# Performance work log

Hardware: AMD Instinct MI355X
Metric: run time of the kernel (lower is better)

Reference implementation:

```python
import jax, jax.numpy as jnp
import numpy as np

LAM = 0.43
IN_DIM = 256
BATCH = 512


def _persistence_pairs(D):
    """0-dim persistence pairs via Kruskal-style union-find (matches torch code).
    D: [n, n] numpy distance matrix. Returns [n-1, 2] int array of MST edges."""
    n = D.shape[0]
    parent = np.arange(n)

    def find(u):
        root = u
        while parent[root] != root:
            root = parent[root]
        while parent[u] != root:  # path compression
            parent[u], u = root, parent[u]
        return root

    iu, ju = np.triu_indices(n)  # includes diagonal, like triu_indices_from
    w = D[iu, ju]
    order = np.argsort(w, kind='stable')
    pairs = []
    for e in order:
        u, v = int(iu[e]), int(ju[e])
        ru, rv = find(u), find(v)
        if ru == rv:
            continue
        if ru > rv:
            parent[rv] = ru  # merge(v, u)
        else:
            parent[ru] = rv  # merge(u, v)
        pairs.append((u, v) if u < v else (v, u))
    return np.asarray(pairs, dtype=np.int64)  # exactly n-1 edges


def _pdist(x):
    # torch.norm(x[:, None] - x, dim=2, p=2)
    return jnp.linalg.norm(x[:, None, :] - x[None, :, :], axis=-1)


def setup_inputs() -> dict:
    key = jax.random.key(0)
    ks = jax.random.split(key, 16)
    d = IN_DIM
    dims = [(d, d // 2), (d // 2, d // 4), (d // 4, 2), (2, d // 4), (d // 4, d // 2), (d // 2, d)]
    inp = {
        'x': jax.random.normal(ks[0], (BATCH, d), dtype=jnp.float32),
        'label': jax.random.randint(ks[1], (BATCH,), 0, 10),
    }
    names = ['1', '2', 'm', '3', '4', '5']
    for i, (nm, (din, dout)) in enumerate(zip(names, dims)):
        s = 1.0 / np.sqrt(din)
        inp['W' + nm] = jax.random.uniform(ks[2 + 2 * i], (din, dout), minval=-s, maxval=s, dtype=jnp.float32)
        inp['b' + nm] = jax.random.uniform(ks[3 + 2 * i], (dout,), minval=-s, maxval=s, dtype=jnp.float32)
    inp['latent_norm'] = jnp.ones((1,), dtype=jnp.float32)
    return inp


def reference(x, label, W1, b1, W2, b2, Wm, bm, W3, b3, W4, b4, W5, b5, latent_norm):
    # Encoder
    h1 = jax.nn.relu(x @ W1 + b1)
    h2 = jax.nn.relu(h1 @ W2 + b2)
    lat = h2 @ Wm + bm  # [B, 2]

    # normalized pairwise distance matrices
    xd = _pdist(x)
    xd = xd / xd.max()  # 2D-input branch
    ld = _pdist(lat) / latent_norm[0]

    # Decoder
    h3 = jax.nn.relu(lat @ W3 + b3)
    h4 = jax.nn.relu(h3 @ W4 + b4)
    xr = h4 @ W5 + b5
    ae_loss = jnp.mean((x - xr) ** 2)

    # persistence pairs (detached / host computation, as in the torch code)
    p1 = _persistence_pairs(np.asarray(jax.device_get(xd)))
    p2 = _persistence_pairs(np.asarray(jax.device_get(ld)))

    sig1 = xd[p1[:, 0], p1[:, 1]]
    sig1_2 = ld[p1[:, 0], p1[:, 1]]
    sig2 = ld[p2[:, 0], p2[:, 1]]
    sig2_1 = xd[p2[:, 0], p2[:, 1]]
    topo = jnp.sum((sig1 - sig1_2) ** 2) + jnp.sum((sig2 - sig2_1) ** 2)

    loss = ae_loss + LAM * topo / float(x.shape[0])
    return loss
```

## Files before the change

kernel.cpp:

```cpp
#include <hip/hip_runtime.h>
#include <math.h>

#define N      512
#define DIN    256
#define LAM    0.43f
#define MAGIC  0x4D535431u
#define NBW    64
#define PAD(j) ((j) + (((j) >> 6) << 2))

#define OFF_LDREADY 4
#define OFF_T0READY 5
#define OFF_T0BITS  6
#define OFF_BLKMAX  8
#define OFF_AEPART  128
#define OFF_LAT     1024
#define OFF_XD      2048
#define OFF_LD      (2048 + 262144)
#define OFF_CAND    526336
#define OFF_GCOMP   (OFF_CAND + 2048)
#define OFF_GNC     (OFF_GCOMP + 1024)
#define OFF_DBAR    (OFF_GNC + 16)
#define OFF_SBAR    (OFF_DBAR + 32)
#define OFF_LDBAR   (OFF_SBAR + 1280)

__device__ __forceinline__ unsigned ld_acq(unsigned* p) {
    return __hip_atomic_load(p, __ATOMIC_ACQUIRE, __HIP_MEMORY_SCOPE_AGENT);
}
__device__ __forceinline__ void st_rel(unsigned* p, unsigned v) {
    __hip_atomic_store(p, v, __ATOMIC_RELEASE, __HIP_MEMORY_SCOPE_AGENT);
}
__device__ __forceinline__ unsigned ld_rlx(unsigned* p) {
    return __hip_atomic_load(p, __ATOMIC_RELAXED, __HIP_MEMORY_SCOPE_AGENT);
}
__device__ __forceinline__ void st_rlx(unsigned* p, unsigned v) {
    __hip_atomic_store(p, v, __ATOMIC_RELAXED, __HIP_MEMORY_SCOPE_AGENT);
}
__device__ __forceinline__ unsigned long long ld64_rlx(unsigned long long* p) {
    return __hip_atomic_load(p, __ATOMIC_RELAXED, __HIP_MEMORY_SCOPE_AGENT);
}
__device__ __forceinline__ void st64_rlx(unsigned long long* p, unsigned long long v) {
    __hip_atomic_store(p, v, __ATOMIC_RELAXED, __HIP_MEMORY_SCOPE_AGENT);
}
__device__ __forceinline__ void spin_magic(unsigned* p) {
    while (ld_acq(p) != MAGIC) __builtin_amdgcn_s_sleep(1);
}

__global__ __launch_bounds__(256) void fused_mlp_pdistx_kernel(
    const float* __restrict__ x,
    const float* __restrict__ W1, const float* __restrict__ b1,
    const float* __restrict__ W2, const float* __restrict__ b2,
    const float* __restrict__ Wm, const float* __restrict__ bm,
    const float* __restrict__ W3, const float* __restrict__ b3,
    const float* __restrict__ W4, const float* __restrict__ b4,
    const float* __restrict__ W5, const float* __restrict__ b5,
    float* __restrict__ lat_out, float* __restrict__ ae_part,
    float* __restrict__ xd, float* __restrict__ blkmax)
{
    const int tid = threadIdx.x;

    if (blockIdx.x < 512) {
        __shared__ float xs[256];
        __shared__ float h1[128];
        __shared__ float h2[64];
        __shared__ float latv[2];
        __shared__ float h3[64];
        __shared__ float h4[128];
        __shared__ float red[4];

        const int row = blockIdx.x;
        xs[tid] = x[(size_t)row * DIN + tid];
        __syncthreads();

        if (tid < 128) {
            float s = b1[tid];
            for (int k = 0; k < 256; ++k) s = fmaf(xs[k], W1[k * 128 + tid], s);
            h1[tid] = fmaxf(s, 0.f);
        }
        __syncthreads();

        if (tid < 64) {
            float s = b2[tid];
            for (int k = 0; k < 128; ++k) s = fmaf(h1[k], W2[k * 64 + tid], s);
            h2[tid] = fmaxf(s, 0.f);
        }
        __syncthreads();

        if (tid < 2) {
            float s = bm[tid];
            for (int k = 0; k < 64; ++k) s = fmaf(h2[k], Wm[k * 2 + tid], s);
            latv[tid] = s;
            lat_out[(size_t)row * 2 + tid] = s;
        }
        __syncthreads();

        if (tid < 64) {
            float s = b3[tid];
            s = fmaf(latv[0], W3[tid], s);
            s = fmaf(latv[1], W3[64 + tid], s);
            h3[tid] = fmaxf(s, 0.f);
        }
        __syncthreads();

        if (tid < 128) {
            float s = b4[tid];
            for (int k = 0; k < 64; ++k) s = fmaf(h3[k], W4[k * 128 + tid], s);
            h4[tid] = fmaxf(s, 0.f);
        }
        __syncthreads();

        float s = b5[tid];
        for (int k = 0; k < 128; ++k) s = fmaf(h4[k], W5[k * 256 + tid], s);
        float diff = xs[tid] - s;
        float a = diff * diff;

        #pragma unroll
        for (int m = 1; m < 64; m <<= 1) a += __shfl_xor(a, m, 64);
        if ((tid & 63) == 0) red[tid >> 6] = a;
        __syncthreads();
        if (tid == 0) ae_part[row] = red[0] + red[1] + red[2] + red[3];
    } else {
        __shared__ float As[32][65];
        __shared__ float Bs[32][65];
        __shared__ float red2[4];

        const int bid = blockIdx.x - 512;
        const int bi = bid & 7, bj = bid >> 3;
        const int i0 = bi * 64, j0 = bj * 64;
        const int ty = tid >> 4, tx = tid & 15;

        float acc[4][4];
        #pragma unroll
        for (int i = 0; i < 4; ++i)
            #pragma unroll
            for (int j = 0; j < 4; ++j) acc[i][j] = 0.f;

        for (int kk = 0; kk < DIN; kk += 32) {
            #pragma unroll
            for (int s = tid; s < 512; s += 256) {
                int r = s >> 3, c4 = (s & 7) << 2;
                float4 va = *(const float4*)(x + (size_t)(i0 + r) * DIN + kk + c4);
                As[c4 + 0][r] = va.x; As[c4 + 1][r] = va.y;
                As[c4 + 2][r] = va.z; As[c4 + 3][r] = va.w;
                float4 vb = *(const float4*)(x + (size_t)(j0 + r) * DIN + kk + c4);
                Bs[c4 + 0][r] = vb.x; Bs[c4 + 1][r] = vb.y;
                Bs[c4 + 2][r] = vb.z; Bs[c4 + 3][r] = vb.w;
            }
            __syncthreads();
            #pragma unroll 8
            for (int k = 0; k < 32; ++k) {
                float a[4], b[4];
                #pragma unroll
                for (int i = 0; i < 4; ++i) a[i] = As[k][ty + 16 * i];
                #pragma unroll
                for (int j = 0; j < 4; ++j) b[j] = Bs[k][tx + 16 * j];
                #pragma unroll
                for (int i = 0; i < 4; ++i)
                    #pragma unroll
                    for (int j = 0; j < 4; ++j) {
                        float d = a[i] - b[j];
                        acc[i][j] = fmaf(d, d, acc[i][j]);
                    }
            }
            __syncthreads();
        }

        float lmax = 0.f;
        #pragma unroll
        for (int i = 0; i < 4; ++i)
            #pragma unroll
            for (int j = 0; j < 4; ++j) {
                float dd = sqrtf(acc[i][j]);
                int r = i0 + ty + 16 * i, c = j0 + tx + 16 * j;
                xd[(size_t)r * N + c] = dd;
                lmax = fmaxf(lmax, dd);
            }

        #pragma unroll
        for (int m = 32; m >= 1; m >>= 1) lmax = fmaxf(lmax, __shfl_xor(lmax, m, 64));
        if ((tid & 63) == 0) red2[tid >> 6] = lmax;
        __syncthreads();
        if (tid == 0)
            blkmax[bid] = fmaxf(fmaxf(red2[0], red2[1]), fmaxf(red2[2], red2[3]));
    }
}

__global__ __launch_bounds__(256) void mst_boruvka_kernel(
    const float* __restrict__ xd, float* __restrict__ ld,
    const float* __restrict__ lat, const float* __restrict__ latent_norm,
    const float* __restrict__ blkmax, const float* __restrict__ ae_part,
    float* __restrict__ wsf, float* __restrict__ out)
{
    __shared__ __align__(16) unsigned comp_p[544];
    __shared__ unsigned comp_a[512];
    __shared__ unsigned long long cval[512];
    __shared__ int tgt[512];
    __shared__ unsigned short eu[512], ev[512];
    __shared__ float ew[512];
    __shared__ float latx[512], laty[512];
    __shared__ float s_red[4];
    __shared__ float s_xdm;
    __shared__ int s_ecnt;
    __shared__ unsigned s_nc;

    const int tid = threadIdx.x;
    const int blk = blockIdx.x;
    const int m   = blk >> 6;
    const int wb  = blk & 63;
    const bool leader = (wb == 0);

    unsigned* ldready = (unsigned*)(wsf + OFF_LDREADY);
    unsigned* t0ready = (unsigned*)(wsf + OFF_T0READY);
    unsigned* t0bits  = (unsigned*)(wsf + OFF_T0BITS);
    unsigned long long* cand = (unsigned long long*)(wsf + OFF_CAND) + (size_t)m * 512;
    unsigned* gcomp = (unsigned*)(wsf + OFF_GCOMP) + (size_t)m * 512;
    unsigned* gnc   = (unsigned*)(wsf + OFF_GNC) + m;
    unsigned* dbar  = (unsigned*)(wsf + OFF_DBAR) + (size_t)m * 16;
    unsigned* sbar  = (unsigned*)(wsf + OFF_SBAR) + (size_t)m * 640;
    unsigned* ldbar = (unsigned*)(wsf + OFF_LDBAR);

    const float* Dm = m ? ld : xd;
    const float* Om = m ? xd : ld;

    if (m == 1) {
        for (int i = tid; i < 512; i += 256) {
            latx[i] = lat[2 * i + 0];
            laty[i] = lat[2 * i + 1];
        }
        __syncthreads();
        const int r0 = wb << 3;
        for (int q = tid; q < 1024; q += 256) {
            int rr = r0 + (q >> 7);
            int j  = (q & 127) << 2;
            float xi = latx[rr], yi = laty[rr];
            float dx0 = xi - latx[j + 0], dy0 = yi - laty[j + 0];
            float dx1 = xi - latx[j + 1], dy1 = yi - laty[j + 1];
            float dx2 = xi - latx[j + 2], dy2 = yi - laty[j + 2];
            float dx3 = xi - latx[j + 3], dy3 = yi - laty[j + 3];
            float4 o;
            o.x = sqrtf(fmaf(dx0, dx0, dy0 * dy0));
            o.y = sqrtf(fmaf(dx1, dx1, dy1 * dy1));
            o.z = sqrtf(fmaf(dx2, dx2, dy2 * dy2));
            o.w = sqrtf(fmaf(dx3, dx3, dy3 * dy3));
            *(float4*)(ld + (size_t)rr * N + j) = o;
        }
        __syncthreads();
        if (tid == 0) st_rel(&ldbar[wb], MAGIC);
        if (tid < 64) spin_magic(&ldbar[tid]);
        __syncthreads();
        if (leader && tid == 0) st_rel(ldready, MAGIC);
    }

    if (leader) {
        for (int i = tid; i < 512; i += 256) comp_a[i] = (unsigned)i;
        if (tid == 0) s_ecnt = 0;
        for (int i = tid; i < 512; i += 256) st64_rlx(&cand[i], ~0ULL);
        __syncthreads();
        if (tid == 0) st_rel(&dbar[0], MAGIC);
    }
    if (tid == 0) spin_magic(&dbar[0]);
    __syncthreads();

    for (int p = 0; p < 9; ++p) {
        if (p > 0) {
            if (tid == 0) { spin_magic(&dbar[p]); s_nc = ld_rlx(gnc); }
            __syncthreads();
            if (s_nc == 1) break;
            for (int i = tid; i < 512; i += 256)
                comp_p[PAD(i)] = ld_rlx(&gcomp[i]);
            __syncthreads();
        }

        const int r  = (wb << 3) + (tid >> 5);
        const int c0 = (tid & 31) << 4;
        const unsigned cv = (p == 0) ? (unsigned)r : comp_p[PAD(r)];
        const float4* rp = (const float4*)(Dm + (size_t)r * N + c0);
        const int4*   cp = (const int4*)&comp_p[PAD(c0)];
        unsigned long long bk = ~0ULL;
        #pragma unroll
        for (int c = 0; c < 4; ++c) {
            float4 f = rp[c];
            int jb = c0 + 4 * c;
            unsigned j0c, j1c, j2c, j3c;
            if (p == 0) { j0c = jb; j1c = jb + 1; j2c = jb + 2; j3c = jb + 3; }
            else { int4 cc = cp[c]; j0c = cc.x; j1c = cc.y; j2c = cc.z; j3c = cc.w; }
            unsigned long long k;
            k = ((unsigned long long)__float_as_uint(f.x) << 18)
              | ((unsigned long long)r << 9) | (unsigned)(jb + 0);
            if (j0c != cv && k < bk) bk = k;
            k = ((unsigned long long)__float_as_uint(f.y) << 18)
              | ((unsigned long long)r << 9) | (unsigned)(jb + 1);
            if (j1c != cv && k < bk) bk = k;
            k = ((unsigned long long)__float_as_uint(f.z) << 18)
              | ((unsigned long long)r << 9) | (unsigned)(jb + 2);
            if (j2c != cv && k < bk) bk = k;
            k = ((unsigned long long)__float_as_uint(f.w) << 18)
              | ((unsigned long long)r << 9) | (unsigned)(jb + 3);
            if (j3c != cv && k < bk) bk = k;
        }
        #pragma unroll
        for (int mm = 1; mm <= 16; mm <<= 1) {
            unsigned long long o = __shfl_xor(bk, mm, 64);
            if (o < bk) bk = o;
        }
        if ((tid & 31) == 0 && bk != ~0ULL)
            atomicMin(&cand[cv], bk);
        __syncthreads();
        if (tid == 0) st_rel(&sbar[p * 64 + wb], MAGIC);

        if (leader) {
            if (tid < 64) spin_magic(&sbar[p * 64 + tid]);
            __syncthreads();
            for (int i = tid; i < 512; i += 256) cval[i] = ld64_rlx(&cand[i]);
            __syncthreads();
            for (int i = tid; i < 512; i += 256) {
                int t = -1;
                if (comp_a[i] == (unsigned)i && cval[i] != ~0ULL)
                    t = (int)comp_a[cval[i] & 511];
                tgt[i] = t;
            }
            __syncthreads();
            for (int i = tid; i < 512; i += 256) {
                int s = tgt[i];
                if (s >= 0 && !(tgt[s] == i && i > s)) {
                    comp_a[i] = (unsigned)s;
                    int e = atomicAdd(&s_ecnt, 1);
                    unsigned long long c = cval[i];
                    eu[e] = (unsigned short)((c >> 9) & 511);
                    ev[e] = (unsigned short)(c & 511);
                    ew[e] = __uint_as_float((unsigned)(c >> 18));
                }
            }
            __syncthreads();
            for (int dd = 0; dd < 9; ++dd) {
                unsigned a = comp_a[comp_a[tid]];
                unsigned b = comp_a[comp_a[tid + 256]];
                __syncthreads();
                comp_a[tid] = a; comp_a[tid + 256] = b;
                __syncthreads();
            }
            const int nc = 512 - s_ecnt;
            for (int i = tid; i < 512; i += 256) {
                st_rlx(&gcomp[i], comp_a[i]);
                st64_rlx(&cand[i], ~0ULL);
            }
            if (tid == 0) st_rlx(gnc, (unsigned)nc);
            __syncthreads();
            if (tid == 0) st_rel(&dbar[p + 1], MAGIC);
            if (nc == 1) break;
        }
    }

    if (leader) {
        if (tid < 64) {
            float mx = blkmax[tid];
            #pragma unroll
            for (int mm = 32; mm >= 1; mm >>= 1)
                mx = fmaxf(mx, __shfl_xor(mx, mm, 64));
            if (tid == 0) s_xdm = mx;
        }
        __syncthreads();
        const float xdm = s_xdm;
        const float lnv = latent_norm[0];
        const float sD = (m == 0) ? 1.f / xdm : 1.f / lnv;
        const float sO = (m == 0) ? 1.f / lnv : 1.f / xdm;

        if (m == 0) {
            if (tid == 0) spin_magic(ldready);
            __syncthreads();
        }

        const int ne = s_ecnt;
        float acc = 0.f;
        for (int i = tid; i < ne; i += 256) {
            float de = ew[i];
            float oe = Om[(size_t)eu[i] * N + ev[i]];
            float c = sD * de - sO * oe;
            acc = fmaf(c, c, acc);
        }
        #pragma unroll
        for (int mm = 32; mm >= 1; mm >>= 1) acc += __shfl_xor(acc, mm, 64);
        if ((tid & 63) == 0) s_red[tid >> 6] = acc;
        __syncthreads();

        if (m == 0) {
            if (tid == 0) {
                float t0 = s_red[0] + s_red[1] + s_red[2] + s_red[3];
                st_rlx(t0bits, __float_as_uint(t0));
                st_rel(t0ready, MAGIC);
            }
        } else {
            float t1 = 0.f;
            if (tid == 0) t1 = s_red[0] + s_red[1] + s_red[2] + s_red[3];
            __syncthreads();
            float a = ae_part[tid] + ae_part[tid + 256];
            #pragma unroll
            for (int mm = 32; mm >= 1; mm >>= 1) a += __shfl_xor(a, mm, 64);
            if ((tid & 63) == 0) s_red[tid >> 6] = a;
            __syncthreads();
            if (tid == 0) {
                float ae = s_red[0] + s_red[1] + s_red[2] + s_red[3];
                spin_magic(t0ready);
                float t0 = __uint_as_float(ld_rlx(t0bits));
                out[0] = ae * (1.f / (float)(N * DIN))
                       + (LAM * (t0 + t1)) * (1.f / (float)N);
            }
        }
    }
}

extern "C" void kernel_launch(void* const* d_in, const int* in_sizes, int n_in,
                              void* d_out, int out_size, void* d_ws, size_t ws_size,
                              hipStream_t stream) {
    const float* x   = (const float*)d_in[0];
    const float* W1  = (const float*)d_in[2];
    const float* b1  = (const float*)d_in[3];
    const float* W2  = (const float*)d_in[4];
    const float* b2  = (const float*)d_in[5];
    const float* Wm  = (const float*)d_in[6];
    const float* bm  = (const float*)d_in[7];
    const float* W3  = (const float*)d_in[8];
    const float* b3  = (const float*)d_in[9];
    const float* W4  = (const float*)d_in[10];
    const float* b4  = (const float*)d_in[11];
    const float* W5  = (const float*)d_in[12];
    const float* b5  = (const float*)d_in[13];
    const float* latent_norm = (const float*)d_in[14];

    float* ws      = (float*)d_ws;
    float* blkmax  = ws + OFF_BLKMAX;
    float* ae_part = ws + OFF_AEPART;
    float* lat     = ws + OFF_LAT;
    float* xd      = ws + OFF_XD;
    float* ld      = ws + OFF_LD;

    fused_mlp_pdistx_kernel<<<576, 256, 0, stream>>>(
        x, W1, b1, W2, b2, Wm, bm, W3, b3, W4, b4, W5, b5,
        lat, ae_part, xd, blkmax);
    mst_boruvka_kernel<<<128, 256, 0, stream>>>(
        xd, ld, lat, latent_norm, blkmax, ae_part, ws, (float*)d_out);
}
```

Before: 174.6 us.

## Replicate Boruvka merge step in every block to drop leader round-trip barrier

```diff
diff --git a/kernel.cpp b/kernel.cpp
--- a/kernel.cpp
+++ b/kernel.cpp
@@ -5,7 +5,6 @@
 #define DIN    256
 #define LAM    0.43f
 #define MAGIC  0x4D535431u
-#define NBW    64
 #define PAD(j) ((j) + (((j) >> 6) << 2))
 
 #define OFF_LDREADY 4
@@ -17,11 +16,7 @@
 #define OFF_XD      2048
 #define OFF_LD      (2048 + 262144)
 #define OFF_CAND    526336
-#define OFF_GCOMP   (OFF_CAND + 2048)
-#define OFF_GNC     (OFF_GCOMP + 1024)
-#define OFF_DBAR    (OFF_GNC + 16)
-#define OFF_SBAR    (OFF_DBAR + 32)
-#define OFF_LDBAR   (OFF_SBAR + 1280)
+#define OFF_BAR     (OFF_CAND + 18432)
 
 __device__ __forceinline__ unsigned ld_acq(unsigned* p) {
     return __hip_atomic_load(p, __ATOMIC_ACQUIRE, __HIP_MEMORY_SCOPE_AGENT);
@@ -31,9 +26,6 @@
 }
 __device__ __forceinline__ unsigned ld_rlx(unsigned* p) {
     return __hip_atomic_load(p, __ATOMIC_RELAXED, __HIP_MEMORY_SCOPE_AGENT);
-}
-__device__ __forceinline__ void st_rlx(unsigned* p, unsigned v) {
-    __hip_atomic_store(p, v, __ATOMIC_RELAXED, __HIP_MEMORY_SCOPE_AGENT);
 }
 __device__ __forceinline__ unsigned long long ld64_rlx(unsigned long long* p) {
     return __hip_atomic_load(p, __ATOMIC_RELAXED, __HIP_MEMORY_SCOPE_AGENT);
@@ -190,8 +182,8 @@
     const float* __restrict__ blkmax, const float* __restrict__ ae_part,
     float* __restrict__ wsf, float* __restrict__ out)
 {
-    __shared__ __align__(16) unsigned comp_p[544];
     __shared__ unsigned comp_a[512];
+    __shared__ __align__(16) unsigned comp_s[544];
     __shared__ unsigned long long cval[512];
     __shared__ int tgt[512];
     __shared__ unsigned short eu[512], ev[512];
@@ -200,7 +192,6 @@
     __shared__ float s_red[4];
     __shared__ float s_xdm;
     __shared__ int s_ecnt;
-    __shared__ unsigned s_nc;
 
     const int tid = threadIdx.x;
     const int blk = blockIdx.x;
@@ -211,12 +202,9 @@
     unsigned* ldready = (unsigned*)(wsf + OFF_LDREADY);
     unsigned* t0ready = (unsigned*)(wsf + OFF_T0READY);
     unsigned* t0bits  = (unsigned*)(wsf + OFF_T0BITS);
-    unsigned long long* cand = (unsigned long long*)(wsf + OFF_CAND) + (size_t)m * 512;
-    unsigned* gcomp = (unsigned*)(wsf + OFF_GCOMP) + (size_t)m * 512;
-    unsigned* gnc   = (unsigned*)(wsf + OFF_GNC) + m;
-    unsigned* dbar  = (unsigned*)(wsf + OFF_DBAR) + (size_t)m * 16;
-    unsigned* sbar  = (unsigned*)(wsf + OFF_SBAR) + (size_t)m * 640;
-    unsigned* ldbar = (unsigned*)(wsf + OFF_LDBAR);
+    unsigned long long* candm =
+        (unsigned long long*)(wsf + OFF_CAND) + (size_t)m * 9 * 512;
+    unsigned* bar = (unsigned*)(wsf + OFF_BAR) + (size_t)m * 640;
 
     const float* Dm = m ? ld : xd;
     const float* Om = m ? xd : ld;
@@ -243,167 +231,154 @@
             o.w = sqrtf(fmaf(dx3, dx3, dy3 * dy3));
             *(float4*)(ld + (size_t)rr * N + j) = o;
         }
-        __syncthreads();
-        if (tid == 0) st_rel(&ldbar[wb], MAGIC);
-        if (tid < 64) spin_magic(&ldbar[tid]);
-        __syncthreads();
-        if (leader && tid == 0) st_rel(ldready, MAGIC);
-    }
-
-    if (leader) {
-        for (int i = tid; i < 512; i += 256) comp_a[i] = (unsigned)i;
-        if (tid == 0) s_ecnt = 0;
-        for (int i = tid; i < 512; i += 256) st64_rlx(&cand[i], ~0ULL);
-        __syncthreads();
-        if (tid == 0) st_rel(&dbar[0], MAGIC);
-    }
-    if (tid == 0) spin_magic(&dbar[0]);
+    }
+
+    for (int i = tid; i < 72; i += 256)
+        st64_rlx(&candm[(size_t)wb * 72 + i], ~0ULL);
+
+    for (int i = tid; i < 512; i += 256) {
+        comp_a[i] = (unsigned)i;
+        comp_s[PAD(i)] = (unsigned)i;
+    }
+    if (tid == 0) s_ecnt = 0;
+
     __syncthreads();
-
-    for (int p = 0; p < 9; ++p) {
-        if (p > 0) {
-            if (tid == 0) { spin_magic(&dbar[p]); s_nc = ld_rlx(gnc); }
+    if (tid == 0) st_rel(&bar[wb], MAGIC);
+    if (tid < 64) spin_magic(&bar[tid]);
+    __syncthreads();
+    if (m == 1 && leader && tid == 0) st_rel(ldready, MAGIC);
+
+    int nc = 512;
+    for (int p = 0; p < 9 && nc > 1; ++p) {
+        unsigned long long* cand = candm + (size_t)p * 512;
+
+        {
+            const int r  = (wb << 3) + (tid >> 5);
+            const int c0 = (tid & 31) << 4;
+            const unsigned cv = comp_s[PAD(r)];
+            const float4* rp = (const float4*)(Dm + (size_t)r * N + c0);
+            unsigned long long bk = ~0ULL;
+            #pragma unroll
+            for (int c = 0; c < 4; ++c) {
+                float4 f = rp[c];
+                int jb = c0 + 4 * c;
+                int4 cc = *(const int4*)&comp_s[PAD(jb)];
+                unsigned long long k;
+                k = ((unsigned long long)__float_as_uint(f.x) << 18)
+                  | ((unsigned long long)r << 9) | (unsigned)(jb + 0);
+                if ((unsigned)cc.x != cv && k < bk) bk = k;
+                k = ((unsigned long long)__float_as_uint(f.y) << 18)
+                  | ((unsigned long long)r << 9) | (unsigned)(jb + 1);
+                if ((unsigned)cc.y != cv && k < bk) bk = k;
+                k = ((unsigned long long)__float_as_uint(f.z) << 18)
+                  | ((unsigned long long)r << 9) | (unsigned)(jb + 2);
+                if ((unsigned)cc.z != cv && k < bk) bk = k;
+                k = ((unsigned long long)__float_as_uint(f.w) << 18)
+                  | ((unsigned long long)r << 9) | (unsigned)(jb + 3);
+                if ((unsigned)cc.w != cv && k < bk) bk = k;
+            }
+            #pragma unroll
+            for (int mm = 1; mm <= 16; mm <<= 1) {
+                unsigned long long o = __shfl_xor(bk, mm, 64);
+                if (o < bk) bk = o;
+            }
+            if ((tid & 31) == 0 && bk != ~0ULL)
+                atomicMin(&cand[cv], bk);
+        }
+
+        __syncthreads();
+        if (tid == 0) st_rel(&bar[(p + 1) * 64 + wb], MAGIC);
+        if (tid < 64) spin_magic(&bar[(p + 1) * 64 + tid]);
+        __syncthreads();
+
+        for (int i = tid; i < 512; i += 256) cval[i] = ld64_rlx(&cand[i]);
+        __syncthreads();
+        for (int i = tid; i < 512; i += 256) {
+            int t = -1;
+            if (comp_a[i] == (unsigned)i && cval[i] != ~0ULL)
+                t = (int)comp_a[cval[i] & 511];
+            tgt[i] = t;
+        }
+        __syncthreads();
+        for (int i = tid; i < 512; i += 256) {
+            int s = tgt[i];
+            if (s >= 0 && !(tgt[s] == i && i > s)) {
+                comp_a[i] = (unsigned)s;
+                int e = atomicAdd(&s_ecnt, 1);
+                unsigned long long c = cval[i];
+                eu[e] = (unsigned short)((c >> 9) & 511);
+                ev[e] = (unsigned short)(c & 511);
+                ew[e] = __uint_as_float((unsigned)(c >> 18));
+            }
+        }
+        __syncthreads();
+        for (int dd = 0; dd < 9; ++dd) {
+            unsigned a = comp_a[comp_a[tid]];
+            unsigned b = comp_a[comp_a[tid + 256]];
             __syncthreads();
-            if (s_nc == 1) break;
-            for (int i = tid; i < 512; i += 256)
-                comp_p[PAD(i)] = ld_rlx(&gcomp[i]);
+            comp_a[tid] = a; comp_a[tid + 256] = b;
             __syncthreads();
         }
-
-        const int r  = (wb << 3) + (tid >> 5);
-        const int c0 = (tid & 31) << 4;
-        const unsigned cv = (p == 0) ? (unsigned)r : comp_p[PAD(r)];
-        const float4* rp = (const float4*)(Dm + (size_t)r * N + c0);
-        const int4*   cp = (const int4*)&comp_p[PAD(c0)];
-        unsigned long long bk = ~0ULL;
-        #pragma unroll
-        for (int c = 0; c < 4; ++c) {
-            float4 f = rp[c];
-            int jb = c0 + 4 * c;
-            unsigned j0c, j1c, j2c, j3c;
-            if (p == 0) { j0c = jb; j1c = jb + 1; j2c = jb + 2; j3c = jb + 3; }
-            else { int4 cc = cp[c]; j0c = cc.x; j1c = cc.y; j2c = cc.z; j3c = cc.w; }
-            unsigned long long k;
-            k = ((unsigned long long)__float_as_uint(f.x) << 18)
-              | ((unsigned long long)r << 9) | (unsigned)(jb + 0);
-            if (j0c != cv && k < bk) bk = k;
-            k = ((unsigned long long)__float_as_uint(f.y) << 18)
-              | ((unsigned long long)r << 9) | (unsigned)(jb + 1);
-            if (j1c != cv && k < bk) bk = k;
-            k = ((unsigned long long)__float_as_uint(f.z) << 18)
-              | ((unsigned long long)r << 9) | (unsigned)(jb + 2);
-            if (j2c != cv && k < bk) bk = k;
-            k = ((unsigned long long)__float_as_uint(f.w) << 18)
-              | ((unsigned long long)r << 9) | (unsigned)(jb + 3);
-            if (j3c != cv && k < bk) bk = k;
-        }
-        #pragma unroll
-        for (int mm = 1; mm <= 16; mm <<= 1) {
-            unsigned long long o = __shfl_xor(bk, mm, 64);
-            if (o < bk) bk = o;
-        }
-        if ((tid & 31) == 0 && bk != ~0ULL)
-            atomicMin(&cand[cv], bk);
-        __syncthreads();
-        if (tid == 0) st_rel(&sbar[p * 64 + wb], MAGIC);
-
-        if (leader) {
-            if (tid < 64) spin_magic(&sbar[p * 64 + tid]);
-            __syncthreads();
-            for (int i = tid; i < 512; i += 256) cval[i] = ld64_rlx(&cand[i]);
-            __syncthreads();
-            for (int i = tid; i < 512; i += 256) {
-                int t = -1;
-                if (comp_a[i] == (unsigned)i && cval[i] != ~0ULL)
-                    t = (int)comp_a[cval[i] & 511];
-                tgt[i] = t;
-            }
-            __syncthreads();
-            for (int i = tid; i < 512; i += 256) {
-                int s = tgt[i];
-                if (s >= 0 && !(tgt[s] == i && i > s)) {
-                    comp_a[i] = (unsigned)s;
-                    int e = atomicAdd(&s_ecnt, 1);
-                    unsigned long long c = cval[i];
-                    eu[e] = (unsigned short)((c >> 9) & 511);
-                    ev[e] = (unsigned short)(c & 511);
-                    ew[e] = __uint_as_float((unsigned)(c >> 18));
-                }
-            }
-            __syncthreads();
-            for (int dd = 0; dd < 9; ++dd) {
-                unsigned a = comp_a[comp_a[tid]];
-                unsigned b = comp_a[comp_a[tid + 256]];
-                __syncthreads();
-                comp_a[tid] = a; comp_a[tid + 256] = b;
-                __syncthreads();
-            }
-            const int nc = 512 - s_ecnt;
-            for (int i = tid; i < 512; i += 256) {
-                st_rlx(&gcomp[i], comp_a[i]);
-                st64_rlx(&cand[i], ~0ULL);
-            }
-            if (tid == 0) st_rlx(gnc, (unsigned)nc);
-            __syncthreads();
-            if (tid == 0) st_rel(&dbar[p + 1], MAGIC);
-            if (nc == 1) break;
-        }
-    }
-
-    if (leader) {
-        if (tid < 64) {
-            float mx = blkmax[tid];
-            #pragma unroll
-            for (int mm = 32; mm >= 1; mm >>= 1)
-                mx = fmaxf(mx, __shfl_xor(mx, mm, 64));
-            if (tid == 0) s_xdm = mx;
-        }
-        __syncthreads();
-        const float xdm = s_xdm;
-        const float lnv = latent_norm[0];
-        const float sD = (m == 0) ? 1.f / xdm : 1.f / lnv;
-        const float sO = (m == 0) ? 1.f / lnv : 1.f / xdm;
-
-        if (m == 0) {
-            if (tid == 0) spin_magic(ldready);
-            __syncthreads();
-        }
-
-        const int ne = s_ecnt;
-        float acc = 0.f;
-        for (int i = tid; i < ne; i += 256) {
-            float de = ew[i];
-            float oe = Om[(size_t)eu[i] * N + ev[i]];
-            float c = sD * de - sO * oe;
-            acc = fmaf(c, c, acc);
-        }
-        #pragma unroll
-        for (int mm = 32; mm >= 1; mm >>= 1) acc += __shfl_xor(acc, mm, 64);
-        if ((tid & 63) == 0) s_red[tid >> 6] = acc;
-        __syncthreads();
-
-        if (m == 0) {
-            if (tid == 0) {
-                float t0 = s_red[0] + s_red[1] + s_red[2] + s_red[3];
-                st_rlx(t0bits, __float_as_uint(t0));
-                st_rel(t0ready, MAGIC);
-            }
-        } else {
-            float t1 = 0.f;
-            if (tid == 0) t1 = s_red[0] + s_red[1] + s_red[2] + s_red[3];
-            __syncthreads();
-            float a = ae_part[tid] + ae_part[tid + 256];
-            #pragma unroll
-            for (int mm = 32; mm >= 1; mm >>= 1) a += __shfl_xor(a, mm, 64);
-            if ((tid & 63) == 0) s_red[tid >> 6] = a;
-            __syncthreads();
-            if (tid == 0) {
-                float ae = s_red[0] + s_red[1] + s_red[2] + s_red[3];
-                spin_magic(t0ready);
-                float t0 = __uint_as_float(ld_rlx(t0bits));
-                out[0] = ae * (1.f / (float)(N * DIN))
-                       + (LAM * (t0 + t1)) * (1.f / (float)N);
-            }
+        for (int i = tid; i < 512; i += 256) comp_s[PAD(i)] = comp_a[i];
+        nc = 512 - s_ecnt;
+        __syncthreads();
+    }
+
+    if (!leader) return;
+
+    if (tid < 64) {
+        float mx = blkmax[tid];
+        #pragma unroll
+        for (int mm = 32; mm >= 1; mm >>= 1)
+            mx = fmaxf(mx, __shfl_xor(mx, mm, 64));
+        if (tid == 0) s_xdm = mx;
+    }
+    __syncthreads();
+    const float xdm = s_xdm;
+    const float lnv = latent_norm[0];
+    const float sD = (m == 0) ? 1.f / xdm : 1.f / lnv;
+    const float sO = (m == 0) ? 1.f / lnv : 1.f / xdm;
+
+    if (m == 0) {
+        if (tid == 0) spin_magic(ldready);
+        __syncthreads();
+    }
+
+    const int ne = s_ecnt;
+    float acc = 0.f;
+    for (int i = tid; i < ne; i += 256) {
+        float de = ew[i];
+        float oe = Om[(size_t)eu[i] * N + ev[i]];
+        float c = sD * de - sO * oe;
+        acc = fmaf(c, c, acc);
+    }
+    #pragma unroll
+    for (int mm = 32; mm >= 1; mm >>= 1) acc += __shfl_xor(acc, mm, 64);
+    if ((tid & 63) == 0) s_red[tid >> 6] = acc;
+    __syncthreads();
+
+    if (m == 0) {
+        if (tid == 0) {
+            float t0 = s_red[0] + s_red[1] + s_red[2] + s_red[3];
+            __hip_atomic_store(t0bits, __float_as_uint(t0), __ATOMIC_RELAXED,
+                               __HIP_MEMORY_SCOPE_AGENT);
+            st_rel(t0ready, MAGIC);
+        }
+    } else {
+        float t1 = 0.f;
+        if (tid == 0) t1 = s_red[0] + s_red[1] + s_red[2] + s_red[3];
+        __syncthreads();
+        float a = ae_part[tid] + ae_part[tid + 256];
+        #pragma unroll
+        for (int mm = 32; mm >= 1; mm >>= 1) a += __shfl_xor(a, mm, 64);
+        if ((tid & 63) == 0) s_red[tid >> 6] = a;
+        __syncthreads();
+        if (tid == 0) {
+            float ae = s_red[0] + s_red[1] + s_red[2] + s_red[3];
+            spin_magic(t0ready);
+            float t0 = __uint_as_float(ld_rlx(t0bits));
+            out[0] = ae * (1.f / (float)(N * DIN))
+                   + (LAM * (t0 + t1)) * (1.f / (float)N);
         }
     }
 }
```

After: 159.2 us. 8.8% less time.
